# Optimization experiments

Hardware: AMD Instinct MI355X
Metric: run time of the kernel (lower is better)

The kernel has to match this reference:

```python
import jax, jax.numpy as jnp
import numpy as np

NBINS = 30
EMBED = 300


def setup_inputs() -> dict:
    key = jax.random.key(0)
    ks = jax.random.split(key, 12)
    B, Q, D = 64, 32, 4096
    inp = {
        "query": jax.random.normal(ks[0], (B, Q, EMBED), dtype=jnp.float32),
        "document": jax.random.normal(ks[1], (B, D, EMBED), dtype=jnp.float32),
        "query_len": jax.random.randint(ks[2], (B,), 0, Q, dtype=jnp.int32),
        # ffn: Linear(30,5) -> Tanh -> Linear(5,1) -> Tanh -> Linear(1,1) -> Tanh
        "W1": jax.random.normal(ks[3], (5, NBINS), dtype=jnp.float32) * 0.1,
        "b1": jax.random.normal(ks[4], (5,), dtype=jnp.float32) * 0.1,
        "W2": jax.random.normal(ks[5], (1, 5), dtype=jnp.float32) * 0.1,
        "b2": jax.random.normal(ks[6], (1,), dtype=jnp.float32) * 0.1,
        "W3": jax.random.normal(ks[7], (1, 1), dtype=jnp.float32) * 0.1,
        "b3": jax.random.normal(ks[8], (1,), dtype=jnp.float32) * 0.1,
        # gate: Linear(embed_dim, 1)
        "Wg": jax.random.normal(ks[9], (1, EMBED), dtype=jnp.float32) * 0.05,
        "bg": jax.random.normal(ks[10], (1,), dtype=jnp.float32) * 0.05,
    }
    return inp


def _batched_hist(interaction, mask, dtype):
    # interaction: [B, Q, D] cosine sims in [-1, 1]; mask: [B, Q] bool (q < query_len)
    B, Q, D = interaction.shape
    # torch.histc(bins=NBINS, min=-1, max=1): bin = floor((x+1)*NBINS/2), clip top edge
    idx = jnp.clip(jnp.floor((interaction + 1.0) * (NBINS / 2.0)).astype(jnp.int32), 0, NBINS - 1)
    row = jnp.arange(B * Q, dtype=jnp.int32)[:, None]  # [B*Q, 1]
    flat = (row * NBINS + idx.reshape(B * Q, D)).reshape(-1)
    counts = jax.ops.segment_sum(jnp.ones((B * Q * D,), dtype=dtype), flat,
                                 num_segments=B * Q * NBINS)
    counts = counts.reshape(B, Q, NBINS)
    # rows with q >= query_len[b] stay zero in the torch code
    return counts * mask[..., None].astype(dtype)


def reference(query, document, query_len, W1, b1, W2, b2, W3, b3, Wg, bg):
    B, Q, E = query.shape
    qn = query / jnp.linalg.norm(query, axis=2, keepdims=True)
    dn = document / jnp.linalg.norm(document, axis=2, keepdims=True)
    interaction = jnp.einsum('bqe,bde->bqd', qn, dn)  # [B, Q, D]
    mask = jnp.arange(Q, dtype=jnp.int32)[None, :] < query_len[:, None]  # [B, Q]
    h = jnp.log1p(_batched_hist(interaction, mask, query.dtype))  # [B, Q, NBINS]
    z = jnp.tanh(h @ W1.T + b1)
    z = jnp.tanh(z @ W2.T + b2)
    z = jnp.tanh(z @ W3.T + b3)[..., 0]  # [B, Q]
    g = jax.nn.softmax((qn @ Wg.T + bg)[..., 0], axis=1)  # note: torch gates on normalized query
    return jnp.sum(z * g, axis=1)  # [B]
```

## Files before the change

### kernel.cpp

```cpp
#include <hip/hip_runtime.h>
#include <math.h>

#define BB 64
#define QQ 32
#define DD 4096
#define EE 300
#define EPAD 320
#define NB 30
#define WD 64
#define TDB 256
#define NDT (DD/TDB)
#define NCH 10

typedef __attribute__((ext_vector_type(8))) short short8v;
typedef __attribute__((ext_vector_type(4))) float f32x4;

static __device__ __forceinline__ unsigned short f2bf(float x) {
    unsigned int u = __builtin_bit_cast(unsigned int, x);
    u = (u + 0x7FFFu + ((u >> 16) & 1u)) >> 16;
    return (unsigned short)u;
}
static __device__ __forceinline__ float bf2f(unsigned short h) {
    return __builtin_bit_cast(float, (unsigned int)h << 16);
}

__global__ __launch_bounds__(64) void drmm_prep(const float* __restrict__ query,
                                                const float* __restrict__ Wg,
                                                const float* __restrict__ bg,
                                                unsigned short* __restrict__ qh,
                                                unsigned short* __restrict__ ql,
                                                float* __restrict__ glog) {
    const int row  = blockIdx.x;
    const int lane = threadIdx.x;
    const float* src = query + (size_t)row * EE;
    float ss = 0.f;
    for (int e = lane; e < EE; e += 64) { float x = src[e]; ss += x * x; }
    for (int o = 1; o < 64; o <<= 1) ss += __shfl_xor(ss, o);
    const float inv = 1.0f / sqrtf(ss);
    float gd = 0.f;
    #pragma unroll
    for (int it = 0; it < 5; ++it) {
        int e = it * 64 + lane;
        float x = (e < EE) ? src[e] * inv : 0.f;
        unsigned short h = f2bf(x);
        float lo = x - bf2f(h);
        qh[(size_t)row * EPAD + e] = h;
        ql[(size_t)row * EPAD + e] = f2bf(lo);
        if (e < EE) gd += x * Wg[e];
    }
    for (int o = 1; o < 64; o <<= 1) gd += __shfl_xor(gd, o);
    if (lane == 0) glog[row] = gd + bg[0];
}

__global__ __launch_bounds__(256, 4) void drmm_main(const float* __restrict__ doc,
                                                    const int* __restrict__ qlen,
                                                    const unsigned short* __restrict__ qh,
                                                    const unsigned short* __restrict__ ql,
                                                    int* __restrict__ ghist) {
    __shared__ int s_hist[QQ][32];

    const int b   = blockIdx.x >> 4;
    const int dt  = blockIdx.x & 15;
    const int len = qlen[b];
    if (len == 0) return;

    const int tid = threadIdx.x;
    const int wv  = tid >> 6;
    const int l15 = tid & 15;
    const int l4  = (tid >> 4) & 3;
    const int nqt = (len > 16) ? 2 : 1;

    for (int s = tid; s < QQ * 32; s += 256) ((int*)s_hist)[s] = 0;

    const float* drow0 = doc + (size_t)(b * DD + dt * TDB + wv * WD + l15) * EE;
    const unsigned short* qhb = qh + ((size_t)b * QQ + l15) * EPAD + l4 * 8;
    const unsigned short* qlb = ql + ((size_t)b * QQ + l15) * EPAD + l4 * 8;

    f32x4 acc[2][4];
    #pragma unroll
    for (int qt = 0; qt < 2; ++qt)
        #pragma unroll
        for (int t = 0; t < 4; ++t) acc[qt][t] = (f32x4){0.f, 0.f, 0.f, 0.f};
    float ssq[4] = {0.f, 0.f, 0.f, 0.f};

    const int kw = l4 * 8;

    for (int c = 0; c < NCH; ++c) {
        const int kb = c * 32 + kw;
        const int k1 = (kb     < EE) ? kb     : 0;
        const int k2 = (kb + 4 < EE) ? kb + 4 : 0;

        f32x4 v[4][2];
        #pragma unroll
        for (int t = 0; t < 4; ++t) {
            const float* rp = drow0 + (size_t)t * 16 * EE;
            v[t][0] = *(const f32x4*)(rp + k1);
            v[t][1] = *(const f32x4*)(rp + k2);
        }
        short8v ah0 = *(const short8v*)(qhb + c * 32);
        short8v al0 = *(const short8v*)(qlb + c * 32);
        short8v ah1 = {}, al1 = {};
        if (nqt > 1) {
            ah1 = *(const short8v*)(qhb + 16 * EPAD + c * 32);
            al1 = *(const short8v*)(qlb + 16 * EPAD + c * 32);
        }

        const bool r1 = (kb < EE), r2 = (kb + 4 < EE);

        #pragma unroll
        for (int t = 0; t < 4; ++t) {
            const f32x4 v0 = v[t][0], v1 = v[t][1];
            if (r1) ssq[t] += v0.x * v0.x + v0.y * v0.y + v0.z * v0.z + v0.w * v0.w;
            if (r2) ssq[t] += v1.x * v1.x + v1.y * v1.y + v1.z * v1.z + v1.w * v1.w;

            short8v bhi, blo;
            #pragma unroll
            for (int j = 0; j < 4; ++j) {
                unsigned short h0 = f2bf(v0[j]);
                unsigned short h1 = f2bf(v1[j]);
                bhi[j]     = (short)h0;
                bhi[j + 4] = (short)h1;
                blo[j]     = (short)f2bf(v0[j] - bf2f(h0));
                blo[j + 4] = (short)f2bf(v1[j] - bf2f(h1));
            }
            acc[0][t] = __builtin_amdgcn_mfma_f32_16x16x32_bf16(ah0, bhi, acc[0][t], 0, 0, 0);
            acc[0][t] = __builtin_amdgcn_mfma_f32_16x16x32_bf16(ah0, blo, acc[0][t], 0, 0, 0);
            acc[0][t] = __builtin_amdgcn_mfma_f32_16x16x32_bf16(al0, bhi, acc[0][t], 0, 0, 0);
            if (nqt > 1) {
                acc[1][t] = __builtin_amdgcn_mfma_f32_16x16x32_bf16(ah1, bhi, acc[1][t], 0, 0, 0);
                acc[1][t] = __builtin_amdgcn_mfma_f32_16x16x32_bf16(ah1, blo, acc[1][t], 0, 0, 0);
                acc[1][t] = __builtin_amdgcn_mfma_f32_16x16x32_bf16(al1, bhi, acc[1][t], 0, 0, 0);
            }
        }
    }

    float rinv[4];
    #pragma unroll
    for (int t = 0; t < 4; ++t) {
        float s = ssq[t];
        s += __shfl_xor(s, 16);
        s += __shfl_xor(s, 32);
        rinv[t] = 1.0f / sqrtf(s);
    }

    __syncthreads();

    #pragma unroll
    for (int qt = 0; qt < 2; ++qt) {
        #pragma unroll
        for (int r = 0; r < 4; ++r) {
            const int q = qt * 16 + l4 * 4 + r;
            if (q < len) {
                #pragma unroll
                for (int t = 0; t < 4; ++t) {
                    float sim = acc[qt][t][r] * rinv[t];
                    int bin = (int)floorf((sim + 1.0f) * 15.0f);
                    bin = bin < 0 ? 0 : (bin > 29 ? 29 : bin);
                    atomicAdd(&s_hist[q][bin], 1);
                }
            }
        }
    }
    __syncthreads();

    for (int s = tid; s < QQ * NB; s += 256) {
        const int q = s / NB, bin = s % NB;
        int tot = s_hist[q][bin];
        if (tot) atomicAdd(&ghist[((size_t)b * QQ + q) * NB + bin], tot);
    }
}

__global__ __launch_bounds__(64) void drmm_final(const int* __restrict__ ghist,
                                                 const float* __restrict__ glog,
                                                 const float* __restrict__ W1,
                                                 const float* __restrict__ b1,
                                                 const float* __restrict__ W2,
                                                 const float* __restrict__ b2,
                                                 const float* __restrict__ W3,
                                                 const float* __restrict__ b3,
                                                 float* __restrict__ out) {
    const int b = blockIdx.x;
    const int lane = threadIdx.x;
    float z = 0.f, lg = -1e30f;
    if (lane < QQ) {
        const int* hrow = ghist + ((size_t)b * QQ + lane) * NB;
        float h[NB];
        #pragma unroll
        for (int v = 0; v < NB; ++v) h[v] = log1pf((float)hrow[v]);
        float t1[5];
        #pragma unroll
        for (int u = 0; u < 5; ++u) {
            float s = b1[u];
            #pragma unroll
            for (int v = 0; v < NB; ++v) s += W1[u * NB + v] * h[v];
            t1[u] = tanhf(s);
        }
        float s2 = b2[0];
        #pragma unroll
        for (int u = 0; u < 5; ++u) s2 += W2[u] * t1[u];
        z = tanhf(W3[0] * tanhf(s2) + b3[0]);
        lg = glog[b * QQ + lane];
    }
    float m = lg;
    for (int o = 16; o >= 1; o >>= 1) m = fmaxf(m, __shfl_xor(m, o));
    float e = (lane < QQ) ? expf(lg - m) : 0.f;
    float s = e;
    for (int o = 16; o >= 1; o >>= 1) s += __shfl_xor(s, o);
    float w = z * (e / s);
    for (int o = 16; o >= 1; o >>= 1) w += __shfl_xor(w, o);
    if (lane == 0) out[b] = w;
}

extern "C" void kernel_launch(void* const* d_in, const int* in_sizes, int n_in,
                              void* d_out, int out_size, void* d_ws, size_t ws_size,
                              hipStream_t stream) {
    const float* query = (const float*)d_in[0];
    const float* doc   = (const float*)d_in[1];
    const int*   qlen  = (const int*)d_in[2];
    const float* W1    = (const float*)d_in[3];
    const float* b1    = (const float*)d_in[4];
    const float* W2    = (const float*)d_in[5];
    const float* b2    = (const float*)d_in[6];
    const float* W3    = (const float*)d_in[7];
    const float* b3    = (const float*)d_in[8];
    const float* Wg    = (const float*)d_in[9];
    const float* bg    = (const float*)d_in[10];
    float* out = (float*)d_out;

    unsigned short* qh = (unsigned short*)d_ws;
    unsigned short* ql = qh + (size_t)BB * QQ * EPAD;
    float* glog = (float*)(ql + (size_t)BB * QQ * EPAD);
    int*   hist = (int*)(glog + BB * QQ);

    hipMemsetAsync(hist, 0, (size_t)BB * QQ * NB * sizeof(int), stream);
    hipLaunchKernelGGL(drmm_prep, dim3(BB * QQ), dim3(64), 0, stream,
                       query, Wg, bg, qh, ql, glog);
    hipLaunchKernelGGL(drmm_main, dim3(BB * NDT), dim3(256), 0, stream,
                       doc, qlen, qh, ql, hist);
    hipLaunchKernelGGL(drmm_final, dim3(BB), dim3(64), 0, stream,
                       hist, glog, W1, b1, W2, b2, W3, b3, out);
}
```

Baseline: 112.6 us.

## Double-buffer doc and query tiles in LDS via async global_load_lds

The main kernel now stages document rows and query hi/lo fragments into XOR-swizzled, double-buffered LDS using direct global-to-LDS loads, so the next K chunk's loads overlap the current chunk's MFMAs. Each block covers 128 documents instead of 256, which doubles the grid, and the histogram reuses the LDS doc buffer. The separate hipMemsetAsync is dropped and the histogram is zeroed inside the prep kernel instead. The cost is two barriers per chunk and hand-tuned vmcnt waits that are fragile.

```diff
diff --git a/kernel.cpp b/kernel.cpp
--- a/kernel.cpp
+++ b/kernel.cpp
@@ -7,9 +7,9 @@
 #define EE 300
 #define EPAD 320
 #define NB 30
-#define WD 64
-#define TDB 256
+#define TDB 128
 #define NDT (DD/TDB)
+#define KC 32
 #define NCH 10
 
 typedef __attribute__((ext_vector_type(8))) short short8v;
@@ -29,9 +29,11 @@
                                                 const float* __restrict__ bg,
                                                 unsigned short* __restrict__ qh,
                                                 unsigned short* __restrict__ ql,
-                                                float* __restrict__ glog) {
+                                                float* __restrict__ glog,
+                                                int* __restrict__ ghist) {
     const int row  = blockIdx.x;
     const int lane = threadIdx.x;
+    if (lane < NB) ghist[(size_t)row * NB + lane] = 0;
     const float* src = query + (size_t)row * EE;
     float ss = 0.f;
     for (int e = lane; e < EE; e += 64) { float x = src[e]; ss += x * x; }
@@ -57,59 +59,100 @@
                                                     const unsigned short* __restrict__ qh,
                                                     const unsigned short* __restrict__ ql,
                                                     int* __restrict__ ghist) {
-    __shared__ int s_hist[QQ][32];
-
-    const int b   = blockIdx.x >> 4;
-    const int dt  = blockIdx.x & 15;
-    const int len = qlen[b];
+    __shared__ __align__(16) float s_doc[2][TDB * KC];
+    __shared__ __align__(16) unsigned short s_qh[2][QQ * KC];
+    __shared__ __align__(16) unsigned short s_ql[2][QQ * KC];
+
+    const int b   = blockIdx.x >> 5;
+    const int dt  = blockIdx.x & 31;
+    const int len = __builtin_amdgcn_readfirstlane(qlen[b]);
     if (len == 0) return;
 
     const int tid = threadIdx.x;
     const int wv  = tid >> 6;
+    const int td  = tid & 63;
     const int l15 = tid & 15;
     const int l4  = (tid >> 4) & 3;
     const int nqt = (len > 16) ? 2 : 1;
 
-    for (int s = tid; s < QQ * 32; s += 256) ((int*)s_hist)[s] = 0;
-
-    const float* drow0 = doc + (size_t)(b * DD + dt * TDB + wv * WD + l15) * EE;
-    const unsigned short* qhb = qh + ((size_t)b * QQ + l15) * EPAD + l4 * 8;
-    const unsigned short* qlb = ql + ((size_t)b * QQ + l15) * EPAD + l4 * 8;
-
-    f32x4 acc[2][4];
+    const float* docb = doc + ((size_t)b * DD + dt * TDB) * EE;
+    const unsigned short* qhb = qh + (size_t)b * QQ * EPAD;
+    const unsigned short* qlb = ql + (size_t)b * QQ * EPAD;
+
+    auto STAGE = [&](int c, int buf) {
+        #pragma unroll
+        for (int i = 0; i < 4; ++i) {
+            int S  = i * 256 + tid;
+            int r  = S >> 3;
+            int lg = (S & 7) ^ (r & 7);
+            int kk = c * KC + 4 * lg;
+            if (kk >= EE) kk = 0;
+            __builtin_amdgcn_global_load_lds(
+                (const __attribute__((address_space(1))) void*)(docb + (size_t)r * EE + kk),
+                (__attribute__((address_space(3))) void*)&s_doc[buf][(i * 256 + wv * 64) * 4],
+                16, 0, 0);
+        }
+        if (wv < 2) {
+            int s  = wv * 64 + td;
+            int q  = s >> 2;
+            int lg = (s & 3) ^ (q & 3);
+            __builtin_amdgcn_global_load_lds(
+                (const __attribute__((address_space(1))) void*)
+                    (qhb + (size_t)q * EPAD + c * KC + 8 * lg),
+                (__attribute__((address_space(3))) void*)&s_qh[buf][wv * 512],
+                16, 0, 0);
+        } else {
+            int s  = (wv - 2) * 64 + td;
+            int q  = s >> 2;
+            int lg = (s & 3) ^ (q & 3);
+            __builtin_amdgcn_global_load_lds(
+                (const __attribute__((address_space(1))) void*)
+                    (qlb + (size_t)q * EPAD + c * KC + 8 * lg),
+                (__attribute__((address_space(3))) void*)&s_ql[buf][(wv - 2) * 512],
+                16, 0, 0);
+        }
+    };
+
+    STAGE(0, 0);
+
+    f32x4 acc[2][2];
     #pragma unroll
     for (int qt = 0; qt < 2; ++qt)
         #pragma unroll
-        for (int t = 0; t < 4; ++t) acc[qt][t] = (f32x4){0.f, 0.f, 0.f, 0.f};
-    float ssq[4] = {0.f, 0.f, 0.f, 0.f};
-
-    const int kw = l4 * 8;
-
+        for (int t = 0; t < 2; ++t) acc[qt][t] = (f32x4){0.f, 0.f, 0.f, 0.f};
+    float ssq[2] = {0.f, 0.f};
+
+    int cur = 0;
     for (int c = 0; c < NCH; ++c) {
-        const int kb = c * 32 + kw;
-        const int k1 = (kb     < EE) ? kb     : 0;
-        const int k2 = (kb + 4 < EE) ? kb + 4 : 0;
-
-        f32x4 v[4][2];
-        #pragma unroll
-        for (int t = 0; t < 4; ++t) {
-            const float* rp = drow0 + (size_t)t * 16 * EE;
-            v[t][0] = *(const f32x4*)(rp + k1);
-            v[t][1] = *(const f32x4*)(rp + k2);
-        }
-        short8v ah0 = *(const short8v*)(qhb + c * 32);
-        short8v al0 = *(const short8v*)(qlb + c * 32);
-        short8v ah1 = {}, al1 = {};
-        if (nqt > 1) {
-            ah1 = *(const short8v*)(qhb + 16 * EPAD + c * 32);
-            al1 = *(const short8v*)(qlb + 16 * EPAD + c * 32);
-        }
-
+        if (c + 1 < NCH) {
+            STAGE(c + 1, cur ^ 1);
+            asm volatile("s_waitcnt vmcnt(5)" ::: "memory");
+        } else {
+            asm volatile("s_waitcnt vmcnt(0)" ::: "memory");
+        }
+        __builtin_amdgcn_s_barrier();
+
+        short8v ah[2], al[2];
+        #pragma unroll
+        for (int qt = 0; qt < 2; ++qt) {
+            if (qt < nqt) {
+                const int qrow = qt * 16 + l15;
+                const int p = l4 ^ (qrow & 3);
+                ah[qt] = *(const short8v*)&s_qh[cur][qrow * KC + p * 8];
+                al[qt] = *(const short8v*)&s_ql[cur][qrow * KC + p * 8];
+            }
+        }
+
+        const int kb = c * KC + l4 * 8;
         const bool r1 = (kb < EE), r2 = (kb + 4 < EE);
 
         #pragma unroll
-        for (int t = 0; t < 4; ++t) {
-            const f32x4 v0 = v[t][0], v1 = v[t][1];
+        for (int t = 0; t < 2; ++t) {
+            const int lrow = wv * 32 + t * 16 + l15;
+            const int p0 = (2 * l4)     ^ (lrow & 7);
+            const int p1 = (2 * l4 + 1) ^ (lrow & 7);
+            const f32x4 v0 = *(const f32x4*)&s_doc[cur][lrow * KC + p0 * 4];
+            const f32x4 v1 = *(const f32x4*)&s_doc[cur][lrow * KC + p1 * 4];
             if (r1) ssq[t] += v0.x * v0.x + v0.y * v0.y + v0.z * v0.z + v0.w * v0.w;
             if (r2) ssq[t] += v1.x * v1.x + v1.y * v1.y + v1.z * v1.z + v1.w * v1.w;
 
@@ -123,26 +166,30 @@
                 blo[j]     = (short)f2bf(v0[j] - bf2f(h0));
                 blo[j + 4] = (short)f2bf(v1[j] - bf2f(h1));
             }
-            acc[0][t] = __builtin_amdgcn_mfma_f32_16x16x32_bf16(ah0, bhi, acc[0][t], 0, 0, 0);
-            acc[0][t] = __builtin_amdgcn_mfma_f32_16x16x32_bf16(ah0, blo, acc[0][t], 0, 0, 0);
-            acc[0][t] = __builtin_amdgcn_mfma_f32_16x16x32_bf16(al0, bhi, acc[0][t], 0, 0, 0);
+            acc[0][t] = __builtin_amdgcn_mfma_f32_16x16x32_bf16(ah[0], bhi, acc[0][t], 0, 0, 0);
+            acc[0][t] = __builtin_amdgcn_mfma_f32_16x16x32_bf16(ah[0], blo, acc[0][t], 0, 0, 0);
+            acc[0][t] = __builtin_amdgcn_mfma_f32_16x16x32_bf16(al[0], bhi, acc[0][t], 0, 0, 0);
             if (nqt > 1) {
-                acc[1][t] = __builtin_amdgcn_mfma_f32_16x16x32_bf16(ah1, bhi, acc[1][t], 0, 0, 0);
-                acc[1][t] = __builtin_amdgcn_mfma_f32_16x16x32_bf16(ah1, blo, acc[1][t], 0, 0, 0);
-                acc[1][t] = __builtin_amdgcn_mfma_f32_16x16x32_bf16(al1, bhi, acc[1][t], 0, 0, 0);
-            }
-        }
-    }
-
-    float rinv[4];
-    #pragma unroll
-    for (int t = 0; t < 4; ++t) {
+                acc[1][t] = __builtin_amdgcn_mfma_f32_16x16x32_bf16(ah[1], bhi, acc[1][t], 0, 0, 0);
+                acc[1][t] = __builtin_amdgcn_mfma_f32_16x16x32_bf16(ah[1], blo, acc[1][t], 0, 0, 0);
+                acc[1][t] = __builtin_amdgcn_mfma_f32_16x16x32_bf16(al[1], bhi, acc[1][t], 0, 0, 0);
+            }
+        }
+        __builtin_amdgcn_s_barrier();
+        cur ^= 1;
+    }
+
+    float rinv[2];
+    #pragma unroll
+    for (int t = 0; t < 2; ++t) {
         float s = ssq[t];
         s += __shfl_xor(s, 16);
         s += __shfl_xor(s, 32);
         rinv[t] = 1.0f / sqrtf(s);
     }
 
+    int* hist = (int*)&s_doc[0][0];
+    for (int s = tid; s < QQ * 32; s += 256) hist[s] = 0;
     __syncthreads();
 
     #pragma unroll
@@ -152,11 +199,11 @@
             const int q = qt * 16 + l4 * 4 + r;
             if (q < len) {
                 #pragma unroll
-                for (int t = 0; t < 4; ++t) {
+                for (int t = 0; t < 2; ++t) {
                     float sim = acc[qt][t][r] * rinv[t];
                     int bin = (int)floorf((sim + 1.0f) * 15.0f);
                     bin = bin < 0 ? 0 : (bin > 29 ? 29 : bin);
-                    atomicAdd(&s_hist[q][bin], 1);
+                    atomicAdd(&hist[q * 32 + bin], 1);
                 }
             }
         }
@@ -165,7 +212,7 @@
 
     for (int s = tid; s < QQ * NB; s += 256) {
         const int q = s / NB, bin = s % NB;
-        int tot = s_hist[q][bin];
+        int tot = hist[q * 32 + bin];
         if (tot) atomicAdd(&ghist[((size_t)b * QQ + q) * NB + bin], tot);
     }
 }
@@ -232,9 +279,8 @@
     float* glog = (float*)(ql + (size_t)BB * QQ * EPAD);
     int*   hist = (int*)(glog + BB * QQ);
 
-    hipMemsetAsync(hist, 0, (size_t)BB * QQ * NB * sizeof(int), stream);
     hipLaunchKernelGGL(drmm_prep, dim3(BB * QQ), dim3(64), 0, stream,
-                       query, Wg, bg, qh, ql, glog);
+                       query, Wg, bg, qh, ql, glog, hist);
     hipLaunchKernelGGL(drmm_main, dim3(BB * NDT), dim3(256), 0, stream,
                        doc, qlen, qh, ql, hist);
     hipLaunchKernelGGL(drmm_final, dim3(BB), dim3(64), 0, stream,
```

New measurement: 94.90 us (median of 2 runs). -15.7%, faster.
